# Kernel tuning notes

Hardware: AMD Instinct MI355X
Metric: run time of the kernel (lower is better)

The kernel has to match this reference:

```python
import jax, jax.numpy as jnp
import numpy as np

D_MODEL = 1024
EXPAND = 2
D_INNER = D_MODEL * EXPAND  # 2048
C = 8
B, T = 4, 2048


def setup_inputs() -> dict:
    key = jax.random.key(0)
    ks = jax.random.split(key, 8)
    x = jax.random.normal(ks[0], (B, T, D_MODEL), jnp.float32)
    # omega init: uniform in [a, b] per the torch code
    a = np.log(1.0 / np.exp(np.log(0.999) / C) - 1.0)
    b = np.log(1.0 / np.exp(np.log(0.9) / C) - 1.0)
    omega = (a + (b - a) * jax.random.uniform(ks[1], (1, 1, D_INNER))).astype(jnp.float32)
    s = 0.02
    Win = (jax.random.normal(ks[2], (2 * D_INNER, D_MODEL)) * s).astype(jnp.float32)   # in_proj, no bias
    Wl = (jax.random.normal(ks[3], (D_INNER, D_INNER)) * s).astype(jnp.float32)        # lambda_proj weight
    bl = jnp.zeros((D_INNER,), jnp.float32)                                            # lambda_proj bias
    Wv = (jax.random.normal(ks[4], (D_INNER, D_INNER)) * s).astype(jnp.float32)        # mixer householder-vector proj
    bv = jnp.zeros((D_INNER,), jnp.float32)
    Wout = (jax.random.normal(ks[5], (D_MODEL, D_INNER)) * s).astype(jnp.float32)      # out_proj, no bias
    return dict(x=x, omega=omega, Win=Win, Wl=Wl, bl=bl, Wv=Wv, bv=bv, Wout=Wout)


def reference(x, omega, Win, Wl, bl, Wv, bv, Wout):
    # in_proj then split into (x, z)
    xz = jnp.einsum('btd,ed->bte', x, Win)              # [B,T,2*D_INNER]
    xi, z = jnp.split(xz, 2, axis=-1)                   # each [B,T,D_INNER]
    # lambda gate (computed for all timesteps at once)
    log_lam = -C * jax.nn.softplus(omega) * jax.nn.sigmoid(jnp.einsum('bti,ji->btj', xi, Wl) + bl)
    lam = jnp.exp(log_lam)                              # [B,T,D_INNER]
    # Householder (rank-1, identity activation) mixer vectors, hoisted out of the scan
    v = jnp.einsum('bti,ji->btj', xi, Wv) + bv          # [B,T,D_INNER]

    h0 = xi[:, 0]                                       # [B,D_INNER]

    def step(h_prev, inp):
        x_t, v_t, lam_t = inp
        vh = jnp.sum(v_t * h_prev, axis=-1, keepdims=True)
        vv = jnp.sum(v_t * v_t, axis=-1, keepdims=True)
        Qh = h_prev - 2.0 * v_t * (vh / vv)             # Householder reflection of h
        h = lam_t * Qh + (1.0 - lam_t) * x_t
        return h, h

    xs = (jnp.swapaxes(xi[:, 1:], 0, 1),                # [T-1,B,D_INNER]
          jnp.swapaxes(v[:, 1:], 0, 1),
          jnp.swapaxes(lam[:, 1:], 0, 1))
    _, hs = jax.lax.scan(step, h0, xs)                  # [T-1,B,D_INNER]
    h = jnp.concatenate([h0[:, None], jnp.swapaxes(hs, 0, 1)], axis=1)  # [B,T,D_INNER]

    return jnp.einsum('bti,di->btd', jax.nn.silu(z) * h, Wout)
```

## Files before the change

kernel.cpp:

```cpp
#include <hip/hip_runtime.h>
#include <cstdint>
#include <cstddef>

typedef unsigned short u16;
typedef __attribute__((ext_vector_type(8))) short s8v;
typedef __attribute__((ext_vector_type(4))) float f4v;
typedef __attribute__((ext_vector_type(2))) float f32x2;

#define D_MODEL 1024
#define D_INNER 2048
#define BT      8192
#define TLEN    2048
#define NBATCH  4

struct alignas(8) U16x4 { u16 x, y, z, w; };

__device__ __forceinline__ u16 f2bf(float f) {
  union { float f; unsigned u; } c; c.f = f;
  unsigned r = c.u + 0x7FFFu + ((c.u >> 16) & 1u);
  return (u16)(r >> 16);
}
__device__ __forceinline__ float bf2f(u16 b) {
  union { unsigned u; float f; } c; c.u = ((unsigned)b) << 16;
  return c.f;
}
__device__ __forceinline__ float blo(unsigned u) {
  union { unsigned u; float f; } c; c.u = u << 16; return c.f;
}
__device__ __forceinline__ float bhi(unsigned u) {
  union { unsigned u; float f; } c; c.u = u & 0xffff0000u; return c.f;
}
__device__ __forceinline__ unsigned pkbf(float lo, float hi) {
  union { float f; unsigned u; } a, b; a.f = lo; b.f = hi;
#if __has_builtin(__builtin_amdgcn_perm)
  return __builtin_amdgcn_perm(b.u + 0x8000u, a.u + 0x8000u, 0x07060302u);
#else
  return ((b.u + 0x8000u) & 0xffff0000u) | ((a.u + 0x8000u) >> 16);
#endif
}

#define DPPADD(x, ctrl) \
  ((x) + __builtin_bit_cast(float, __builtin_amdgcn_update_dpp( \
       0, __builtin_bit_cast(int, (x)), (ctrl), 0xF, 0xF, true)))
__device__ __forceinline__ float wave_sum_dpp(float x) {
  x = DPPADD(x, 0x111);
  x = DPPADD(x, 0x112);
  x = DPPADD(x, 0x114);
  x = DPPADD(x, 0x118);
  x = DPPADD(x, 0x142);
  x = DPPADD(x, 0x143);
  return x;
}

__device__ __forceinline__ void glds16(const u16* g, const u16* lds) {
  __builtin_amdgcn_global_load_lds(
      (const __attribute__((address_space(1))) unsigned int*)(uintptr_t)g,
      (__attribute__((address_space(3))) unsigned int*)(unsigned int)(uintptr_t)lds,
      16, 0, 0);
}

template<int EPI>
__global__ __launch_bounds__(256, 2)
void gemm_nt(const u16* __restrict__ A, const u16* __restrict__ B,
             int M, int N, int K,
             float* __restrict__ Cf, u16* __restrict__ Cb, u16* __restrict__ Cb2,
             const float* __restrict__ bias, const float* __restrict__ sfac,
             const float* __restrict__ bias2)
{
  __shared__ u16 lA[128 * 32];
  __shared__ u16 lB[128 * 32];
  const int tid  = threadIdx.x;
  const int wave = tid >> 6, lane = tid & 63;
  const int wm = wave >> 1, wn = wave & 1;
  const int bm0 = blockIdx.y * 128, bn0 = blockIdx.x * 128;

  const int srow = lane >> 2;
  const int scol = (lane & 3) * 8;
  const u16* pa0 = A + (size_t)(bm0 + wave * 32 + srow) * K + scol;
  const u16* pa1 = pa0 + (size_t)16 * K;
  const u16* pb0 = B + (size_t)(bn0 + wave * 32 + srow) * K + scol;
  const u16* pb1 = pb0 + (size_t)16 * K;
  u16* la0 = lA + (wave * 32) * 32;
  u16* la1 = la0 + 16 * 32;
  u16* lb0 = lB + (wave * 32) * 32;
  u16* lb1 = lb0 + 16 * 32;

  const int fr = lane & 15, kq = lane >> 4;
  const u16* fA = lA + (wm * 64 + fr) * 32 + kq * 8;
  const u16* fB = lB + (wn * 64 + fr) * 32 + kq * 8;

  f4v acc[4][4];
  const f4v zf = {0.f, 0.f, 0.f, 0.f};
  for (int i = 0; i < 4; ++i)
    for (int j = 0; j < 4; ++j)
      acc[i][j] = zf;

  for (int k0 = 0; k0 < K; k0 += 32) {
    glds16(pa0 + k0, la0);
    glds16(pa1 + k0, la1);
    glds16(pb0 + k0, lb0);
    glds16(pb1 + k0, lb1);
    __syncthreads();
    s8v af[4], bfv[4];
#pragma unroll
    for (int i = 0; i < 4; ++i) af[i] = *(const s8v*)(fA + i * 16 * 32);
#pragma unroll
    for (int j = 0; j < 4; ++j) bfv[j] = *(const s8v*)(fB + j * 16 * 32);
#pragma unroll
    for (int i = 0; i < 4; ++i)
#pragma unroll
      for (int j = 0; j < 4; ++j)
        acc[i][j] = __builtin_amdgcn_mfma_f32_16x16x32_bf16(af[i], bfv[j], acc[i][j], 0, 0, 0);
    __syncthreads();
  }

#pragma unroll
  for (int i = 0; i < 4; ++i) {
#pragma unroll
    for (int j = 0; j < 4; ++j) {
#pragma unroll
      for (int r = 0; r < 4; ++r) {
        const int gm = bm0 + wm * 64 + i * 16 + kq * 4 + r;
        const int gn = bn0 + wn * 64 + j * 16 + fr;
        const float val = acc[i][j][r];
        if (EPI == 0) {
          if (gn < D_INNER) {
            Cb[(size_t)gm * D_INNER + gn] = f2bf(val);
          } else {
            const float s = val / (1.f + __expf(-val));
            Cb2[(size_t)gm * D_INNER + (gn - D_INNER)] = f2bf(s);
          }
        } else if (EPI == 4) {
          if (gn < D_INNER) {
            const float pre = val + bias[gn];
            const float sig = 1.f / (1.f + __expf(-pre));
            Cf[(size_t)gm * D_INNER + gn] = __expf(sfac[gn] * sig);
          } else {
            Cb[(size_t)gm * D_INNER + (gn - D_INNER)] = f2bf(val + bias2[gn - D_INNER]);
          }
        } else {
          Cf[(size_t)gm * N + gn] = val;
        }
      }
    }
  }
}

__global__ void conv_bf16_kernel(const float* __restrict__ in, u16* __restrict__ out, int n4)
{
  const int i = blockIdx.x * blockDim.x + threadIdx.x;
  if (i >= n4) return;
  const float4 x = ((const float4*)in)[i];
  U16x4 o; o.x = f2bf(x.x); o.y = f2bf(x.y); o.z = f2bf(x.z); o.w = f2bf(x.w);
  ((U16x4*)out)[i] = o;
}

__global__ void sfac_kernel(const float* __restrict__ omega, float* __restrict__ sfac)
{
  const int i = blockIdx.x * blockDim.x + threadIdx.x;
  if (i < D_INNER) sfac[i] = -8.f * log1pf(expf(omega[i]));
}

__global__ __launch_bounds__(256)
void vscale_kernel(u16* __restrict__ v)
{
  const int row  = blockIdx.x * 4 + (threadIdx.x >> 6);
  const int lane = threadIdx.x & 63;
  uint4* p = (uint4*)(v + (size_t)row * D_INNER + lane * 32);
  uint4 a[4];
#pragma unroll
  for (int i = 0; i < 4; ++i) a[i] = p[i];
  float s = 0.f;
#pragma unroll
  for (int i = 0; i < 4; ++i) {
    const unsigned w[4] = {a[i].x, a[i].y, a[i].z, a[i].w};
#pragma unroll
    for (int j = 0; j < 4; ++j) {
      const float f0 = blo(w[j]), f1 = bhi(w[j]);
      s += f0 * f0 + f1 * f1;
    }
  }
  s += __shfl_down(s, 32); s += __shfl_down(s, 16); s += __shfl_down(s, 8);
  s += __shfl_down(s, 4);  s += __shfl_down(s, 2);  s += __shfl_down(s, 1);
  const float sc = sqrtf(2.f / __shfl(s, 0));
#pragma unroll
  for (int i = 0; i < 4; ++i) {
    const unsigned w[4] = {a[i].x, a[i].y, a[i].z, a[i].w};
    unsigned o[4];
#pragma unroll
    for (int j = 0; j < 4; ++j) o[j] = pkbf(blo(w[j]) * sc, bhi(w[j]) * sc);
    uint4 ov; ov.x = o[0]; ov.y = o[1]; ov.z = o[2]; ov.w = o[3];
    p[i] = ov;
  }
}

__global__ __launch_bounds__(256)
void pairprep_kernel(const u16* __restrict__ vs, const float* __restrict__ lam,
                     const u16* __restrict__ xi, u16* __restrict__ w,
                     f32x2* __restrict__ C12)
{
  const int r = blockIdx.x * 4 + (threadIdx.x >> 6);
  const int lane = threadIdx.x & 63;
  const int b = r >> 10;
  const int t = (r & 1023) * 2;
  const size_t o0 = ((size_t)b * TLEN + t) * D_INNER + (size_t)lane * 32;
  const size_t o1 = o0 + D_INNER;
  const uint4*  pv0 = (const uint4*)(vs + o0);
  const uint4*  pv1 = (const uint4*)(vs + o1);
  const uint4*  px0 = (const uint4*)(xi + o0);
  const float4* pl0 = (const float4*)(lam + o0);
  uint4* pw = (uint4*)(w + (size_t)r * D_INNER + (size_t)lane * 32);
  float c1 = 0.f, c2 = 0.f;
#pragma unroll
  for (int i = 0; i < 4; ++i) {
    const uint4 v0 = pv0[i], v1 = pv1[i], x0 = px0[i];
    const float4 la = pl0[2 * i], lb2 = pl0[2 * i + 1];
    const unsigned v0w[4] = {v0.x, v0.y, v0.z, v0.w};
    const unsigned v1w[4] = {v1.x, v1.y, v1.z, v1.w};
    const unsigned x0w[4] = {x0.x, x0.y, x0.z, x0.w};
    const float lf[8] = {la.x, la.y, la.z, la.w, lb2.x, lb2.y, lb2.z, lb2.w};
    unsigned ow[4];
#pragma unroll
    for (int q = 0; q < 4; ++q) {
      const float va = blo(v0w[q]), vb = bhi(v0w[q]);
      const float ua = blo(v1w[q]), ub = bhi(v1w[q]);
      const float xa = blo(x0w[q]), xb = bhi(x0w[q]);
      ow[q] = pkbf(ua * lf[2 * q], ub * lf[2 * q + 1]);
      c1 += blo(ow[q]) * va + bhi(ow[q]) * vb;
      c2 += ua * (1.f - lf[2 * q]) * xa + ub * (1.f - lf[2 * q + 1]) * xb;
    }
    uint4 o; o.x = ow[0]; o.y = ow[1]; o.z = ow[2]; o.w = ow[3];
    pw[i] = o;
  }
  c1 = wave_sum_dpp(c1);
  c2 = wave_sum_dpp(c2);
  if (lane == 63) { f32x2 cc; cc.x = c1; cc.y = c2; C12[r] = cc; }
}

struct Pair {
  uint4 v0, v1, w, x0, x1, z0, z1;
  float4 l0a, l0b, l1a, l1b;
  f32x2 c;
};

__global__ __launch_bounds__(256, 1)
void scan2_kernel(const u16* __restrict__ xi, const u16* __restrict__ sz,
                  const u16* __restrict__ vs, const float* __restrict__ lam,
                  const u16* __restrict__ whalf, const f32x2* __restrict__ C12,
                  u16* __restrict__ gh)
{
  const int b = blockIdx.x, tid = threadIdx.x;
  const int wave = tid >> 6, lane = tid & 63;
  const size_t base = (size_t)b * TLEN * D_INNER + (size_t)tid * 8;
  const size_t wb0  = (size_t)(b * 1024) * D_INNER + (size_t)tid * 8;
  const int cb0 = b * 1024;
  __shared__ __attribute__((aligned(16))) float rP[2][4], rQ[2][4];

  auto load_pair = [&](int t) {
    Pair p;
    const size_t o0 = base + (size_t)t * D_INNER;
    const size_t o1 = o0 + D_INNER;
    p.v0 = *(const uint4*)(vs + o0);
    p.v1 = *(const uint4*)(vs + o1);
    p.w  = *(const uint4*)(whalf + wb0 + (size_t)(t >> 1) * D_INNER);
    p.x0 = *(const uint4*)(xi + o0);
    p.x1 = *(const uint4*)(xi + o1);
    p.z0 = *(const uint4*)(sz + o0);
    p.z1 = *(const uint4*)(sz + o1);
    const float4* l0p = (const float4*)(lam + o0);
    p.l0a = l0p[0]; p.l0b = l0p[1];
    const float4* l1p = (const float4*)(lam + o1);
    p.l1a = l1p[0]; p.l1b = l1p[1];
    p.c = C12[cb0 + (t >> 1)];
    return p;
  };

  float h[8];
  {
    const uint4 x0 = *(const uint4*)(xi + base);
    const uint4 z0 = *(const uint4*)(sz + base);
    const unsigned xw[4] = {x0.x, x0.y, x0.z, x0.w};
    const unsigned zw[4] = {z0.x, z0.y, z0.z, z0.w};
    unsigned ow[4];
#pragma unroll
    for (int p = 0; p < 4; ++p) {
      h[2*p]   = blo(xw[p]);
      h[2*p+1] = bhi(xw[p]);
      ow[p] = pkbf(blo(zw[p]) * h[2*p], bhi(zw[p]) * h[2*p+1]);
    }
    uint4 out; out.x = ow[0]; out.y = ow[1]; out.z = ow[2]; out.w = ow[3];
    *(uint4*)(gh + base) = out;
  }

  {
    const size_t o = base + D_INNER;
    const uint4 v1v = *(const uint4*)(vs + o);
    const uint4 x1v = *(const uint4*)(xi + o);
    const uint4 z1v = *(const uint4*)(sz + o);
    const float4* lp = (const float4*)(lam + o);
    const float4 la = lp[0], lb2 = lp[1];
    const unsigned vw[4] = {v1v.x, v1v.y, v1v.z, v1v.w};
    float vf[8];
    float P0 = 0.f, P1 = 0.f;
#pragma unroll
    for (int p = 0; p < 4; ++p) {
      vf[2*p]   = blo(vw[p]);
      vf[2*p+1] = bhi(vw[p]);
      P0 = __builtin_fmaf(vf[2*p],   h[2*p],   P0);
      P1 = __builtin_fmaf(vf[2*p+1], h[2*p+1], P1);
    }
    float P = wave_sum_dpp(P0 + P1);
    if (lane == 63) rP[0][wave] = P;
    asm volatile("s_waitcnt lgkmcnt(0)\n\ts_barrier" ::: "memory");
    const float4 sp = *(const float4*)rP[0];
    const float a = (sp.x + sp.y) + (sp.z + sp.w);
    const float lf[8] = {la.x, la.y, la.z, la.w, lb2.x, lb2.y, lb2.z, lb2.w};
    const unsigned xw[4] = {x1v.x, x1v.y, x1v.z, x1v.w};
    const unsigned zw[4] = {z1v.x, z1v.y, z1v.z, z1v.w};
    unsigned ow[4];
#pragma unroll
    for (int p = 0; p < 4; ++p) {
      const float X0 = blo(xw[p]), X1 = bhi(xw[p]);
      const float t0 = __builtin_fmaf(vf[2*p],   -a, h[2*p]);
      const float t1 = __builtin_fmaf(vf[2*p+1], -a, h[2*p+1]);
      h[2*p]   = __builtin_fmaf(lf[2*p],   t0 - X0, X0);
      h[2*p+1] = __builtin_fmaf(lf[2*p+1], t1 - X1, X1);
      ow[p] = pkbf(blo(zw[p]) * h[2*p], bhi(zw[p]) * h[2*p+1]);
    }
    uint4 out; out.x = ow[0]; out.y = ow[1]; out.z = ow[2]; out.w = ow[3];
    *(uint4*)(gh + o) = out;
  }

  auto round = [&](const Pair& p, int t) {
    const int par = (t >> 1) & 1;
    const unsigned vw[4] = {p.v0.x, p.v0.y, p.v0.z, p.v0.w};
    const unsigned ww[4] = {p.w.x, p.w.y, p.w.z, p.w.w};
    float vf[8];
    float P0 = 0.f, P1 = 0.f, Q0 = 0.f, Q1 = 0.f;
#pragma unroll
    for (int q = 0; q < 4; ++q) {
      vf[2*q]   = blo(vw[q]);
      vf[2*q+1] = bhi(vw[q]);
      const float wa = blo(ww[q]), wb = bhi(ww[q]);
      P0 = __builtin_fmaf(vf[2*q],   h[2*q],   P0);
      P1 = __builtin_fmaf(vf[2*q+1], h[2*q+1], P1);
      Q0 = __builtin_fmaf(wa, h[2*q],   Q0);
      Q1 = __builtin_fmaf(wb, h[2*q+1], Q1);
    }
    float P = wave_sum_dpp(P0 + P1);
    float Q = wave_sum_dpp(Q0 + Q1);
    if (lane == 63) { rP[par][wave] = P; rQ[par][wave] = Q; }
    asm volatile("s_waitcnt lgkmcnt(0)\n\ts_barrier" ::: "memory");
    const float4 sp = *(const float4*)rP[par];
    const float4 sq = *(const float4*)rQ[par];
    const float a0 = (sp.x + sp.y) + (sp.z + sp.w);
    const float a1 = __builtin_fmaf(-a0, p.c.x, (sq.x + sq.y) + (sq.z + sq.w) + p.c.y);
    const float lf0[8] = {p.l0a.x, p.l0a.y, p.l0a.z, p.l0a.w,
                          p.l0b.x, p.l0b.y, p.l0b.z, p.l0b.w};
    const float lf1[8] = {p.l1a.x, p.l1a.y, p.l1a.z, p.l1a.w,
                          p.l1b.x, p.l1b.y, p.l1b.z, p.l1b.w};
    const unsigned v1w[4] = {p.v1.x, p.v1.y, p.v1.z, p.v1.w};
    const unsigned xw0[4] = {p.x0.x, p.x0.y, p.x0.z, p.x0.w};
    const unsigned xw1[4] = {p.x1.x, p.x1.y, p.x1.z, p.x1.w};
    const unsigned zw0[4] = {p.z0.x, p.z0.y, p.z0.z, p.z0.w};
    const unsigned zw1[4] = {p.z1.x, p.z1.y, p.z1.z, p.z1.w};
    unsigned ow0[4], ow1[4];
#pragma unroll
    for (int q = 0; q < 4; ++q) {
      const float A0 = blo(xw0[q]), A1 = bhi(xw0[q]);
      const float B0 = blo(xw1[q]), B1 = bhi(xw1[q]);
      float t0 = __builtin_fmaf(vf[2*q],   -a0, h[2*q]);
      float t1 = __builtin_fmaf(vf[2*q+1], -a0, h[2*q+1]);
      t0 = __builtin_fmaf(lf0[2*q],   t0 - A0, A0);
      t1 = __builtin_fmaf(lf0[2*q+1], t1 - A1, A1);
      ow0[q] = pkbf(blo(zw0[q]) * t0, bhi(zw0[q]) * t1);
      const float u0 = __builtin_fmaf(blo(v1w[q]), -a1, t0);
      const float u1 = __builtin_fmaf(bhi(v1w[q]), -a1, t1);
      h[2*q]   = __builtin_fmaf(lf1[2*q],   u0 - B0, B0);
      h[2*q+1] = __builtin_fmaf(lf1[2*q+1], u1 - B1, B1);
      ow1[q] = pkbf(blo(zw1[q]) * h[2*q], bhi(zw1[q]) * h[2*q+1]);
    }
    const size_t oo = base + (size_t)t * D_INNER;
    uint4 o0; o0.x = ow0[0]; o0.y = ow0[1]; o0.z = ow0[2]; o0.w = ow0[3];
    uint4 o1; o1.x = ow1[0]; o1.y = ow1[1]; o1.z = ow1[2]; o1.w = ow1[3];
    *(uint4*)(gh + oo) = o0;
    *(uint4*)(gh + oo + D_INNER) = o1;
  };

  Pair A = load_pair(2);
  __builtin_amdgcn_sched_barrier(0);
  Pair B = load_pair(4);
  __builtin_amdgcn_sched_barrier(0);
  for (int t = 2; t <= 2038; t += 4) {
    Pair An = load_pair(t + 4);
    __builtin_amdgcn_sched_barrier(0);
    round(A, t);
    A = An;
    Pair Bn = load_pair(t + 6);
    __builtin_amdgcn_sched_barrier(0);
    round(B, t + 2);
    B = Bn;
  }
  {
    Pair An = load_pair(2046);
    __builtin_amdgcn_sched_barrier(0);
    round(A, 2042);
    round(B, 2044);
    round(An, 2046);
  }
}

extern "C" void kernel_launch(void* const* d_in, const int* in_sizes, int n_in,
                              void* d_out, int out_size, void* d_ws, size_t ws_size,
                              hipStream_t stream)
{
  const float* x     = (const float*)d_in[0];
  const float* omega = (const float*)d_in[1];
  const float* Win   = (const float*)d_in[2];
  const float* Wl    = (const float*)d_in[3];
  const float* bl    = (const float*)d_in[4];
  const float* Wv    = (const float*)d_in[5];
  const float* bv    = (const float*)d_in[6];
  const float* Wout  = (const float*)d_in[7];
  float* out = (float*)d_out;
  (void)in_sizes; (void)n_in; (void)out_size; (void)ws_size;

  size_t off = 0;
  auto carve = [&](size_t bytes) -> void* {
    void* r = (char*)d_ws + off;
    off += (bytes + 255) & ~(size_t)255;
    return r;
  };
  u16*  x_bf    = (u16*)carve((size_t)BT * D_MODEL * 2);
  u16*  Win_bf  = (u16*)carve((size_t)2 * D_INNER * D_MODEL * 2);
  u16*  Wl_bf   = (u16*)carve((size_t)D_INNER * D_INNER * 2);
  u16*  Wv_bf   = (u16*)carve((size_t)D_INNER * D_INNER * 2);
  u16*  Wout_bf = (u16*)carve((size_t)D_MODEL * D_INNER * 2);
  u16*  xi_bf   = (u16*)carve((size_t)BT * D_INNER * 2);
  u16*  sz_bf   = (u16*)carve((size_t)BT * D_INNER * 2);
  u16*  v_bf    = (u16*)carve((size_t)BT * D_INNER * 2);
  u16*  gh_bf   = (u16*)carve((size_t)BT * D_INNER * 2);
  float* lam    = (float*)carve((size_t)BT * D_INNER * 4);
  float* sfac   = (float*)carve((size_t)D_INNER * 4);
  f32x2* C12    = (f32x2*)carve((size_t)(BT / 2) * 8);
  u16*  whalf   = x_bf;

  conv_bf16_kernel<<<(BT * D_MODEL / 4 + 255) / 256, 256, 0, stream>>>(x, x_bf, BT * D_MODEL / 4);
  conv_bf16_kernel<<<(2 * D_INNER * D_MODEL / 4 + 255) / 256, 256, 0, stream>>>(Win, Win_bf, 2 * D_INNER * D_MODEL / 4);
  conv_bf16_kernel<<<(D_INNER * D_INNER / 4 + 255) / 256, 256, 0, stream>>>(Wl, Wl_bf, D_INNER * D_INNER / 4);
  conv_bf16_kernel<<<(D_INNER * D_INNER / 4 + 255) / 256, 256, 0, stream>>>(Wv, Wv_bf, D_INNER * D_INNER / 4);
  conv_bf16_kernel<<<(D_MODEL * D_INNER / 4 + 255) / 256, 256, 0, stream>>>(Wout, Wout_bf, D_MODEL * D_INNER / 4);
  sfac_kernel<<<(D_INNER + 255) / 256, 256, 0, stream>>>(omega, sfac);

  gemm_nt<0><<<dim3(4096 / 128, BT / 128), 256, 0, stream>>>(
      x_bf, Win_bf, BT, 4096, D_MODEL, nullptr, xi_bf, sz_bf, nullptr, nullptr, nullptr);
  gemm_nt<4><<<dim3(4096 / 128, BT / 128), 256, 0, stream>>>(
      xi_bf, Wl_bf, BT, 4096, D_INNER, lam, v_bf, nullptr, bl, sfac, bv);
  vscale_kernel<<<BT / 4, 256, 0, stream>>>(v_bf);
  pairprep_kernel<<<BT / 2 / 4, 256, 0, stream>>>(v_bf, lam, xi_bf, whalf, C12);
  scan2_kernel<<<NBATCH, 256, 0, stream>>>(xi_bf, sz_bf, v_bf, lam, whalf, C12, gh_bf);
  gemm_nt<3><<<dim3(D_MODEL / 128, BT / 128), 256, 0, stream>>>(
      gh_bf, Wout_bf, BT, D_MODEL, D_INNER, out, nullptr, nullptr, nullptr, nullptr, nullptr);
}
```

Baseline: 1.265 ms.

## Unroll Householder scan to four steps per barrier with precomputed quad coefficients

Replaces the pairwise scan with a four-step blocked recurrence. A prep kernel precomputes the lambda-weighted v vectors and the scalar coupling coefficients for each quad, so the sequential scan needs only one block barrier per four timesteps. The scan block also grows to 512 threads with 4 elements per thread, which makes each step shorter. In exchange the prep kernel does more work and writes three weight rows per quad, and the scan reads more data per step.

Result: slower. 1.472 ms (+16.3%).

```diff
diff --git a/kernel.cpp b/kernel.cpp
--- a/kernel.cpp
+++ b/kernel.cpp
@@ -5,13 +5,14 @@
 typedef unsigned short u16;
 typedef __attribute__((ext_vector_type(8))) short s8v;
 typedef __attribute__((ext_vector_type(4))) float f4v;
-typedef __attribute__((ext_vector_type(2))) float f32x2;
 
 #define D_MODEL 1024
 #define D_INNER 2048
 #define BT      8192
 #define TLEN    2048
 #define NBATCH  4
+#define QSLOT   512
+#define NQUAD   511
 
 struct alignas(8) U16x4 { u16 x, y, z, w; };
 
@@ -19,10 +20,6 @@
   union { float f; unsigned u; } c; c.f = f;
   unsigned r = c.u + 0x7FFFu + ((c.u >> 16) & 1u);
   return (u16)(r >> 16);
-}
-__device__ __forceinline__ float bf2f(u16 b) {
-  union { unsigned u; float f; } c; c.u = ((unsigned)b) << 16;
-  return c.f;
 }
 __device__ __forceinline__ float blo(unsigned u) {
   union { unsigned u; float f; } c; c.u = u << 16; return c.f;
@@ -195,219 +192,262 @@
 }
 
 __global__ __launch_bounds__(256)
-void pairprep_kernel(const u16* __restrict__ vs, const float* __restrict__ lam,
-                     const u16* __restrict__ xi, u16* __restrict__ w,
-                     f32x2* __restrict__ C12)
+void quadprep_kernel(const u16* __restrict__ vs, const float* __restrict__ lam,
+                     const u16* __restrict__ xi, u16* __restrict__ wq,
+                     float4* __restrict__ cf)
 {
   const int r = blockIdx.x * 4 + (threadIdx.x >> 6);
   const int lane = threadIdx.x & 63;
-  const int b = r >> 10;
-  const int t = (r & 1023) * 2;
-  const size_t o0 = ((size_t)b * TLEN + t) * D_INNER + (size_t)lane * 32;
-  const size_t o1 = o0 + D_INNER;
-  const uint4*  pv0 = (const uint4*)(vs + o0);
-  const uint4*  pv1 = (const uint4*)(vs + o1);
-  const uint4*  px0 = (const uint4*)(xi + o0);
-  const float4* pl0 = (const float4*)(lam + o0);
-  uint4* pw = (uint4*)(w + (size_t)r * D_INNER + (size_t)lane * 32);
-  float c1 = 0.f, c2 = 0.f;
+  const int b = r >> 9;
+  const int q = r & (QSLOT - 1);
+  if (q >= NQUAD) return;
+  const int t0 = 4 * q + 1;
+  const size_t e = ((size_t)b * TLEN + t0) * D_INNER + (size_t)lane * 32;
+  u16* w2p = wq + ((size_t)r * 3 + 0) * D_INNER + (size_t)lane * 32;
+  u16* w3p = wq + ((size_t)r * 3 + 1) * D_INNER + (size_t)lane * 32;
+  u16* w4p = wq + ((size_t)r * 3 + 2) * D_INNER + (size_t)lane * 32;
+
+  float c21 = 0, c31 = 0, c32 = 0, c41 = 0, c42 = 0, c43 = 0;
+  float d2 = 0, d3 = 0, d4 = 0;
+
 #pragma unroll
   for (int i = 0; i < 4; ++i) {
-    const uint4 v0 = pv0[i], v1 = pv1[i], x0 = px0[i];
-    const float4 la = pl0[2 * i], lb2 = pl0[2 * i + 1];
-    const unsigned v0w[4] = {v0.x, v0.y, v0.z, v0.w};
+    const size_t o = e + i * 8;
+    const uint4 v1 = *(const uint4*)(vs + o);
+    const uint4 v2 = *(const uint4*)(vs + o + D_INNER);
+    const uint4 v3 = *(const uint4*)(vs + o + 2 * D_INNER);
+    const uint4 v4 = *(const uint4*)(vs + o + 3 * D_INNER);
+    const uint4 x1 = *(const uint4*)(xi + o);
+    const uint4 x2 = *(const uint4*)(xi + o + D_INNER);
+    const uint4 x3 = *(const uint4*)(xi + o + 2 * D_INNER);
+    const float4* l1p = (const float4*)(lam + o);
+    const float4* l2p = (const float4*)(lam + o + D_INNER);
+    const float4* l3p = (const float4*)(lam + o + 2 * D_INNER);
+    const float4 l1a4 = l1p[0], l1b4 = l1p[1];
+    const float4 l2a4 = l2p[0], l2b4 = l2p[1];
+    const float4 l3a4 = l3p[0], l3b4 = l3p[1];
+    const float lf1[8] = {l1a4.x, l1a4.y, l1a4.z, l1a4.w, l1b4.x, l1b4.y, l1b4.z, l1b4.w};
+    const float lf2[8] = {l2a4.x, l2a4.y, l2a4.z, l2a4.w, l2b4.x, l2b4.y, l2b4.z, l2b4.w};
+    const float lf3[8] = {l3a4.x, l3a4.y, l3a4.z, l3a4.w, l3b4.x, l3b4.y, l3b4.z, l3b4.w};
     const unsigned v1w[4] = {v1.x, v1.y, v1.z, v1.w};
-    const unsigned x0w[4] = {x0.x, x0.y, x0.z, x0.w};
-    const float lf[8] = {la.x, la.y, la.z, la.w, lb2.x, lb2.y, lb2.z, lb2.w};
-    unsigned ow[4];
-#pragma unroll
-    for (int q = 0; q < 4; ++q) {
-      const float va = blo(v0w[q]), vb = bhi(v0w[q]);
-      const float ua = blo(v1w[q]), ub = bhi(v1w[q]);
-      const float xa = blo(x0w[q]), xb = bhi(x0w[q]);
-      ow[q] = pkbf(ua * lf[2 * q], ub * lf[2 * q + 1]);
-      c1 += blo(ow[q]) * va + bhi(ow[q]) * vb;
-      c2 += ua * (1.f - lf[2 * q]) * xa + ub * (1.f - lf[2 * q + 1]) * xb;
-    }
-    uint4 o; o.x = ow[0]; o.y = ow[1]; o.z = ow[2]; o.w = ow[3];
-    pw[i] = o;
-  }
-  c1 = wave_sum_dpp(c1);
-  c2 = wave_sum_dpp(c2);
-  if (lane == 63) { f32x2 cc; cc.x = c1; cc.y = c2; C12[r] = cc; }
-}
-
-struct Pair {
-  uint4 v0, v1, w, x0, x1, z0, z1;
-  float4 l0a, l0b, l1a, l1b;
-  f32x2 c;
+    const unsigned v2w[4] = {v2.x, v2.y, v2.z, v2.w};
+    const unsigned v3w[4] = {v3.x, v3.y, v3.z, v3.w};
+    const unsigned v4w[4] = {v4.x, v4.y, v4.z, v4.w};
+    const unsigned x1w[4] = {x1.x, x1.y, x1.z, x1.w};
+    const unsigned x2w[4] = {x2.x, x2.y, x2.z, x2.w};
+    const unsigned x3w[4] = {x3.x, x3.y, x3.z, x3.w};
+    unsigned ow2[4], ow3[4], ow4[4];
+#pragma unroll
+    for (int k = 0; k < 4; ++k) {
+      const float v1a = blo(v1w[k]), v1b = bhi(v1w[k]);
+      const float v2a = blo(v2w[k]), v2b = bhi(v2w[k]);
+      const float v3a = blo(v3w[k]), v3b = bhi(v3w[k]);
+      const float v4a = blo(v4w[k]), v4b = bhi(v4w[k]);
+      const float l1a = lf1[2*k], l1b = lf1[2*k+1];
+      const float l2a = lf2[2*k], l2b = lf2[2*k+1];
+      const float l3a = lf3[2*k], l3b = lf3[2*k+1];
+      const float u1a = (1.f - l1a) * blo(x1w[k]), u1b = (1.f - l1b) * bhi(x1w[k]);
+      const float u2a = (1.f - l2a) * blo(x2w[k]), u2b = (1.f - l2b) * bhi(x2w[k]);
+      const float u3a = (1.f - l3a) * blo(x3w[k]), u3b = (1.f - l3b) * bhi(x3w[k]);
+      const float p2a = v2a * l1a, p2b = v2b * l1b;
+      ow2[k] = pkbf(p2a, p2b);
+      c21 += blo(ow2[k]) * v1a + bhi(ow2[k]) * v1b;
+      d2  += v2a * u1a + v2b * u1b;
+      const float p3a = v3a * l2a, p3b = v3b * l2b;
+      c32 += p3a * v2a + p3b * v2b;
+      d3  += p3a * u1a + p3b * u1b + v3a * u2a + v3b * u2b;
+      const float w3a = p3a * l1a, w3b = p3b * l1b;
+      ow3[k] = pkbf(w3a, w3b);
+      c31 += blo(ow3[k]) * v1a + bhi(ow3[k]) * v1b;
+      const float p4a = v4a * l3a, p4b = v4b * l3b;
+      c43 += p4a * v3a + p4b * v3b;
+      const float q4a = p4a * l2a, q4b = p4b * l2b;
+      c42 += q4a * v2a + q4b * v2b;
+      d4  += q4a * u1a + q4b * u1b + p4a * u2a + p4b * u2b + v4a * u3a + v4b * u3b;
+      const float w4a = q4a * l1a, w4b = q4b * l1b;
+      ow4[k] = pkbf(w4a, w4b);
+      c41 += blo(ow4[k]) * v1a + bhi(ow4[k]) * v1b;
+    }
+    uint4 s2; s2.x = ow2[0]; s2.y = ow2[1]; s2.z = ow2[2]; s2.w = ow2[3];
+    uint4 s3; s3.x = ow3[0]; s3.y = ow3[1]; s3.z = ow3[2]; s3.w = ow3[3];
+    uint4 s4; s4.x = ow4[0]; s4.y = ow4[1]; s4.z = ow4[2]; s4.w = ow4[3];
+    *(uint4*)(w2p + i * 8) = s2;
+    *(uint4*)(w3p + i * 8) = s3;
+    *(uint4*)(w4p + i * 8) = s4;
+  }
+  c21 = wave_sum_dpp(c21); c31 = wave_sum_dpp(c31); c32 = wave_sum_dpp(c32);
+  c41 = wave_sum_dpp(c41); c42 = wave_sum_dpp(c42); c43 = wave_sum_dpp(c43);
+  d2 = wave_sum_dpp(d2); d3 = wave_sum_dpp(d3); d4 = wave_sum_dpp(d4);
+  if (lane == 63) {
+    float4 a; a.x = c21; a.y = c31; a.z = c32; a.w = c41;
+    float4 bq; bq.x = c42; bq.y = c43; bq.z = d2; bq.w = d3;
+    float4 cc; cc.x = d4; cc.y = 0.f; cc.z = 0.f; cc.w = 0.f;
+    cf[(size_t)r * 3 + 0] = a;
+    cf[(size_t)r * 3 + 1] = bq;
+    cf[(size_t)r * 3 + 2] = cc;
+  }
+}
+
+struct Quad {
+  uint2 w2, w3, w4;
+  uint2 v1, v2, v3, v4;
+  uint2 x1, x2, x3, x4;
+  uint2 z1, z2, z3, z4;
+  float4 l1, l2, l3, l4;
+  float4 c0, c1, c2;
 };
 
-__global__ __launch_bounds__(256, 1)
-void scan2_kernel(const u16* __restrict__ xi, const u16* __restrict__ sz,
+__global__ __launch_bounds__(512, 2)
+void scan4_kernel(const u16* __restrict__ xi, const u16* __restrict__ sz,
                   const u16* __restrict__ vs, const float* __restrict__ lam,
-                  const u16* __restrict__ whalf, const f32x2* __restrict__ C12,
+                  const u16* __restrict__ wq, const float4* __restrict__ cf,
                   u16* __restrict__ gh)
 {
   const int b = blockIdx.x, tid = threadIdx.x;
   const int wave = tid >> 6, lane = tid & 63;
-  const size_t base = (size_t)b * TLEN * D_INNER + (size_t)tid * 8;
-  const size_t wb0  = (size_t)(b * 1024) * D_INNER + (size_t)tid * 8;
-  const int cb0 = b * 1024;
-  __shared__ __attribute__((aligned(16))) float rP[2][4], rQ[2][4];
-
-  auto load_pair = [&](int t) {
-    Pair p;
-    const size_t o0 = base + (size_t)t * D_INNER;
-    const size_t o1 = o0 + D_INNER;
-    p.v0 = *(const uint4*)(vs + o0);
-    p.v1 = *(const uint4*)(vs + o1);
-    p.w  = *(const uint4*)(whalf + wb0 + (size_t)(t >> 1) * D_INNER);
-    p.x0 = *(const uint4*)(xi + o0);
-    p.x1 = *(const uint4*)(xi + o1);
-    p.z0 = *(const uint4*)(sz + o0);
-    p.z1 = *(const uint4*)(sz + o1);
-    const float4* l0p = (const float4*)(lam + o0);
-    p.l0a = l0p[0]; p.l0b = l0p[1];
-    const float4* l1p = (const float4*)(lam + o1);
-    p.l1a = l1p[0]; p.l1b = l1p[1];
-    p.c = C12[cb0 + (t >> 1)];
+  const size_t base = (size_t)b * TLEN * D_INNER + (size_t)tid * 4;
+  __shared__ __attribute__((aligned(16))) float sS[2][4][8];
+
+  auto load_quad = [&](int q) {
+    Quad p;
+    const size_t e1 = base + (size_t)(4 * q + 1) * D_INNER;
+    p.v1 = *(const uint2*)(vs + e1);
+    p.v2 = *(const uint2*)(vs + e1 + D_INNER);
+    p.v3 = *(const uint2*)(vs + e1 + 2 * D_INNER);
+    p.v4 = *(const uint2*)(vs + e1 + 3 * D_INNER);
+    p.x1 = *(const uint2*)(xi + e1);
+    p.x2 = *(const uint2*)(xi + e1 + D_INNER);
+    p.x3 = *(const uint2*)(xi + e1 + 2 * D_INNER);
+    p.x4 = *(const uint2*)(xi + e1 + 3 * D_INNER);
+    p.z1 = *(const uint2*)(sz + e1);
+    p.z2 = *(const uint2*)(sz + e1 + D_INNER);
+    p.z3 = *(const uint2*)(sz + e1 + 2 * D_INNER);
+    p.z4 = *(const uint2*)(sz + e1 + 3 * D_INNER);
+    p.l1 = *(const float4*)(lam + e1);
+    p.l2 = *(const float4*)(lam + e1 + D_INNER);
+    p.l3 = *(const float4*)(lam + e1 + 2 * D_INNER);
+    p.l4 = *(const float4*)(lam + e1 + 3 * D_INNER);
+    const size_t wr = ((size_t)(b * QSLOT + q) * 3) * D_INNER + (size_t)tid * 4;
+    p.w2 = *(const uint2*)(wq + wr);
+    p.w3 = *(const uint2*)(wq + wr + D_INNER);
+    p.w4 = *(const uint2*)(wq + wr + 2 * D_INNER);
+    const float4* cp = cf + (size_t)(b * QSLOT + q) * 3;
+    p.c0 = cp[0]; p.c1 = cp[1]; p.c2 = cp[2];
     return p;
   };
 
-  float h[8];
+  float h[4];
   {
-    const uint4 x0 = *(const uint4*)(xi + base);
-    const uint4 z0 = *(const uint4*)(sz + base);
-    const unsigned xw[4] = {x0.x, x0.y, x0.z, x0.w};
-    const unsigned zw[4] = {z0.x, z0.y, z0.z, z0.w};
-    unsigned ow[4];
-#pragma unroll
-    for (int p = 0; p < 4; ++p) {
-      h[2*p]   = blo(xw[p]);
-      h[2*p+1] = bhi(xw[p]);
-      ow[p] = pkbf(blo(zw[p]) * h[2*p], bhi(zw[p]) * h[2*p+1]);
-    }
-    uint4 out; out.x = ow[0]; out.y = ow[1]; out.z = ow[2]; out.w = ow[3];
-    *(uint4*)(gh + base) = out;
-  }
-
+    const uint2 x0 = *(const uint2*)(xi + base);
+    const uint2 z0 = *(const uint2*)(sz + base);
+    h[0] = blo(x0.x); h[1] = bhi(x0.x); h[2] = blo(x0.y); h[3] = bhi(x0.y);
+    uint2 ov;
+    ov.x = pkbf(blo(z0.x) * h[0], bhi(z0.x) * h[1]);
+    ov.y = pkbf(blo(z0.y) * h[2], bhi(z0.y) * h[3]);
+    *(uint2*)(gh + base) = ov;
+  }
+
+  auto step = [&](uint2 vv, float4 lv, uint2 xv, uint2 zv, float s, size_t off) {
+    const float vf[4] = {blo(vv.x), bhi(vv.x), blo(vv.y), bhi(vv.y)};
+    const float xf[4] = {blo(xv.x), bhi(xv.x), blo(xv.y), bhi(xv.y)};
+    const float lf[4] = {lv.x, lv.y, lv.z, lv.w};
+#pragma unroll
+    for (int k = 0; k < 4; ++k) {
+      const float t_ = __builtin_fmaf(vf[k], -s, h[k]);
+      h[k] = __builtin_fmaf(lf[k], t_ - xf[k], xf[k]);
+    }
+    uint2 ov;
+    ov.x = pkbf(blo(zv.x) * h[0], bhi(zv.x) * h[1]);
+    ov.y = pkbf(blo(zv.y) * h[2], bhi(zv.y) * h[3]);
+    *(uint2*)(gh + off) = ov;
+  };
+
+  auto round = [&](const Quad& p, int q) {
+    const int par = q & 1;
+    const float v1f[4] = {blo(p.v1.x), bhi(p.v1.x), blo(p.v1.y), bhi(p.v1.y)};
+    const float w2f[4] = {blo(p.w2.x), bhi(p.w2.x), blo(p.w2.y), bhi(p.w2.y)};
+    const float w3f[4] = {blo(p.w3.x), bhi(p.w3.x), blo(p.w3.y), bhi(p.w3.y)};
+    const float w4f[4] = {blo(p.w4.x), bhi(p.w4.x), blo(p.w4.y), bhi(p.w4.y)};
+    float P1 = 0.f, P2 = 0.f, P3 = 0.f, P4 = 0.f;
+#pragma unroll
+    for (int k = 0; k < 4; ++k) {
+      P1 = __builtin_fmaf(v1f[k], h[k], P1);
+      P2 = __builtin_fmaf(w2f[k], h[k], P2);
+      P3 = __builtin_fmaf(w3f[k], h[k], P3);
+      P4 = __builtin_fmaf(w4f[k], h[k], P4);
+    }
+    P1 = wave_sum_dpp(P1); P2 = wave_sum_dpp(P2);
+    P3 = wave_sum_dpp(P3); P4 = wave_sum_dpp(P4);
+    if (lane == 63) {
+      sS[par][0][wave] = P1; sS[par][1][wave] = P2;
+      sS[par][2][wave] = P3; sS[par][3][wave] = P4;
+    }
+    asm volatile("s_waitcnt lgkmcnt(0)\n\ts_barrier" ::: "memory");
+    float S[4];
+#pragma unroll
+    for (int j = 0; j < 4; ++j) {
+      const float4 pa = *(const float4*)&sS[par][j][0];
+      const float4 pb = *(const float4*)&sS[par][j][4];
+      S[j] = ((pa.x + pa.y) + (pa.z + pa.w)) + ((pb.x + pb.y) + (pb.z + pb.w));
+    }
+    const float c21 = p.c0.x, c31 = p.c0.y, c32 = p.c0.z, c41 = p.c0.w;
+    const float c42 = p.c1.x, c43 = p.c1.y, d2 = p.c1.z, d3 = p.c1.w;
+    const float d4 = p.c2.x;
+    const float s1 = S[0];
+    const float s2 = __builtin_fmaf(-c21, s1, S[1] + d2);
+    const float s3 = __builtin_fmaf(-c32, s2, __builtin_fmaf(-c31, s1, S[2] + d3));
+    const float s4 = __builtin_fmaf(-c43, s3,
+                      __builtin_fmaf(-c42, s2, __builtin_fmaf(-c41, s1, S[3] + d4)));
+    const size_t e1 = base + (size_t)(4 * q + 1) * D_INNER;
+    step(p.v1, p.l1, p.x1, p.z1, s1, e1);
+    step(p.v2, p.l2, p.x2, p.z2, s2, e1 + D_INNER);
+    step(p.v3, p.l3, p.x3, p.z3, s3, e1 + 2 * D_INNER);
+    step(p.v4, p.l4, p.x4, p.z4, s4, e1 + 3 * D_INNER);
+  };
+
+  auto solo = [&](int t, int par) {
+    const size_t o = base + (size_t)t * D_INNER;
+    const uint2 vv = *(const uint2*)(vs + o);
+    const uint2 xv = *(const uint2*)(xi + o);
+    const uint2 zv = *(const uint2*)(sz + o);
+    const float4 lv = *(const float4*)(lam + o);
+    const float vf[4] = {blo(vv.x), bhi(vv.x), blo(vv.y), bhi(vv.y)};
+    float P = 0.f;
+#pragma unroll
+    for (int k = 0; k < 4; ++k) P = __builtin_fmaf(vf[k], h[k], P);
+    P = wave_sum_dpp(P);
+    if (lane == 63) sS[par][0][wave] = P;
+    asm volatile("s_waitcnt lgkmcnt(0)\n\ts_barrier" ::: "memory");
+    const float4 pa = *(const float4*)&sS[par][0][0];
+    const float4 pb = *(const float4*)&sS[par][0][4];
+    const float s = ((pa.x + pa.y) + (pa.z + pa.w)) + ((pb.x + pb.y) + (pb.z + pb.w));
+    step(vv, lv, xv, zv, s, o);
+  };
+
+  Quad A = load_quad(0);
+  __builtin_amdgcn_sched_barrier(0);
+  Quad B = load_quad(1);
+  __builtin_amdgcn_sched_barrier(0);
+  for (int q = 0; q <= 507; q += 2) {
+    Quad An = load_quad(q + 2);
+    __builtin_amdgcn_sched_barrier(0);
+    round(A, q);
+    A = An;
+    Quad Bn = load_quad(q + 3);
+    __builtin_amdgcn_sched_barrier(0);
+    round(B, q + 1);
+    B = Bn;
+  }
   {
-    const size_t o = base + D_INNER;
-    const uint4 v1v = *(const uint4*)(vs + o);
-    const uint4 x1v = *(const uint4*)(xi + o);
-    const uint4 z1v = *(const uint4*)(sz + o);
-    const float4* lp = (const float4*)(lam + o);
-    const float4 la = lp[0], lb2 = lp[1];
-    const unsigned vw[4] = {v1v.x, v1v.y, v1v.z, v1v.w};
-    float vf[8];
-    float P0 = 0.f, P1 = 0.f;
-#pragma unroll
-    for (int p = 0; p < 4; ++p) {
-      vf[2*p]   = blo(vw[p]);
-      vf[2*p+1] = bhi(vw[p]);
-      P0 = __builtin_fmaf(vf[2*p],   h[2*p],   P0);
-      P1 = __builtin_fmaf(vf[2*p+1], h[2*p+1], P1);
-    }
-    float P = wave_sum_dpp(P0 + P1);
-    if (lane == 63) rP[0][wave] = P;
-    asm volatile("s_waitcnt lgkmcnt(0)\n\ts_barrier" ::: "memory");
-    const float4 sp = *(const float4*)rP[0];
-    const float a = (sp.x + sp.y) + (sp.z + sp.w);
-    const float lf[8] = {la.x, la.y, la.z, la.w, lb2.x, lb2.y, lb2.z, lb2.w};
-    const unsigned xw[4] = {x1v.x, x1v.y, x1v.z, x1v.w};
-    const unsigned zw[4] = {z1v.x, z1v.y, z1v.z, z1v.w};
-    unsigned ow[4];
-#pragma unroll
-    for (int p = 0; p < 4; ++p) {
-      const float X0 = blo(xw[p]), X1 = bhi(xw[p]);
-      const float t0 = __builtin_fmaf(vf[2*p],   -a, h[2*p]);
-      const float t1 = __builtin_fmaf(vf[2*p+1], -a, h[2*p+1]);
-      h[2*p]   = __builtin_fmaf(lf[2*p],   t0 - X0, X0);
-      h[2*p+1] = __builtin_fmaf(lf[2*p+1], t1 - X1, X1);
-      ow[p] = pkbf(blo(zw[p]) * h[2*p], bhi(zw[p]) * h[2*p+1]);
-    }
-    uint4 out; out.x = ow[0]; out.y = ow[1]; out.z = ow[2]; out.w = ow[3];
-    *(uint4*)(gh + o) = out;
-  }
-
-  auto round = [&](const Pair& p, int t) {
-    const int par = (t >> 1) & 1;
-    const unsigned vw[4] = {p.v0.x, p.v0.y, p.v0.z, p.v0.w};
-    const unsigned ww[4] = {p.w.x, p.w.y, p.w.z, p.w.w};
-    float vf[8];
-    float P0 = 0.f, P1 = 0.f, Q0 = 0.f, Q1 = 0.f;
-#pragma unroll
-    for (int q = 0; q < 4; ++q) {
-      vf[2*q]   = blo(vw[q]);
-      vf[2*q+1] = bhi(vw[q]);
-      const float wa = blo(ww[q]), wb = bhi(ww[q]);
-      P0 = __builtin_fmaf(vf[2*q],   h[2*q],   P0);
-      P1 = __builtin_fmaf(vf[2*q+1], h[2*q+1], P1);
-      Q0 = __builtin_fmaf(wa, h[2*q],   Q0);
-      Q1 = __builtin_fmaf(wb, h[2*q+1], Q1);
-    }
-    float P = wave_sum_dpp(P0 + P1);
-    float Q = wave_sum_dpp(Q0 + Q1);
-    if (lane == 63) { rP[par][wave] = P; rQ[par][wave] = Q; }
-    asm volatile("s_waitcnt lgkmcnt(0)\n\ts_barrier" ::: "memory");
-    const float4 sp = *(const float4*)rP[par];
-    const float4 sq = *(const float4*)rQ[par];
-    const float a0 = (sp.x + sp.y) + (sp.z + sp.w);
-    const float a1 = __builtin_fmaf(-a0, p.c.x, (sq.x + sq.y) + (sq.z + sq.w) + p.c.y);
-    const float lf0[8] = {p.l0a.x, p.l0a.y, p.l0a.z, p.l0a.w,
-                          p.l0b.x, p.l0b.y, p.l0b.z, p.l0b.w};
-    const float lf1[8] = {p.l1a.x, p.l1a.y, p.l1a.z, p.l1a.w,
-                          p.l1b.x, p.l1b.y, p.l1b.z, p.l1b.w};
-    const unsigned v1w[4] = {p.v1.x, p.v1.y, p.v1.z, p.v1.w};
-    const unsigned xw0[4] = {p.x0.x, p.x0.y, p.x0.z, p.x0.w};
-    const unsigned xw1[4] = {p.x1.x, p.x1.y, p.x1.z, p.x1.w};
-    const unsigned zw0[4] = {p.z0.x, p.z0.y, p.z0.z, p.z0.w};
-    const unsigned zw1[4] = {p.z1.x, p.z1.y, p.z1.z, p.z1.w};
-    unsigned ow0[4], ow1[4];
-#pragma unroll
-    for (int q = 0; q < 4; ++q) {
-      const float A0 = blo(xw0[q]), A1 = bhi(xw0[q]);
-      const float B0 = blo(xw1[q]), B1 = bhi(xw1[q]);
-      float t0 = __builtin_fmaf(vf[2*q],   -a0, h[2*q]);
-      float t1 = __builtin_fmaf(vf[2*q+1], -a0, h[2*q+1]);
-      t0 = __builtin_fmaf(lf0[2*q],   t0 - A0, A0);
-      t1 = __builtin_fmaf(lf0[2*q+1], t1 - A1, A1);
-      ow0[q] = pkbf(blo(zw0[q]) * t0, bhi(zw0[q]) * t1);
-      const float u0 = __builtin_fmaf(blo(v1w[q]), -a1, t0);
-      const float u1 = __builtin_fmaf(bhi(v1w[q]), -a1, t1);
-      h[2*q]   = __builtin_fmaf(lf1[2*q],   u0 - B0, B0);
-      h[2*q+1] = __builtin_fmaf(lf1[2*q+1], u1 - B1, B1);
-      ow1[q] = pkbf(blo(zw1[q]) * h[2*q], bhi(zw1[q]) * h[2*q+1]);
-    }
-    const size_t oo = base + (size_t)t * D_INNER;
-    uint4 o0; o0.x = ow0[0]; o0.y = ow0[1]; o0.z = ow0[2]; o0.w = ow0[3];
-    uint4 o1; o1.x = ow1[0]; o1.y = ow1[1]; o1.z = ow1[2]; o1.w = ow1[3];
-    *(uint4*)(gh + oo) = o0;
-    *(uint4*)(gh + oo + D_INNER) = o1;
-  };
-
-  Pair A = load_pair(2);
-  __builtin_amdgcn_sched_barrier(0);
-  Pair B = load_pair(4);
-  __builtin_amdgcn_sched_barrier(0);
-  for (int t = 2; t <= 2038; t += 4) {
-    Pair An = load_pair(t + 4);
+    Quad An = load_quad(510);
     __builtin_amdgcn_sched_barrier(0);
-    round(A, t);
-    A = An;
-    Pair Bn = load_pair(t + 6);
-    __builtin_amdgcn_sched_barrier(0);
-    round(B, t + 2);
-    B = Bn;
-  }
-  {
-    Pair An = load_pair(2046);
-    __builtin_amdgcn_sched_barrier(0);
-    round(A, 2042);
-    round(B, 2044);
-    round(An, 2046);
-  }
+    round(A, 508);
+    round(B, 509);
+    round(An, 510);
+  }
+  solo(2045, 1);
+  solo(2046, 0);
+  solo(2047, 1);
 }
 
 extern "C" void kernel_launch(void* const* d_in, const int* in_sizes, int n_in,
@@ -442,8 +482,8 @@
   u16*  gh_bf   = (u16*)carve((size_t)BT * D_INNER * 2);
   float* lam    = (float*)carve((size_t)BT * D_INNER * 4);
   float* sfac   = (float*)carve((size_t)D_INNER * 4);
-  f32x2* C12    = (f32x2*)carve((size_t)(BT / 2) * 8);
-  u16*  whalf   = x_bf;
+  float4* cf    = (float4*)carve((size_t)NBATCH * QSLOT * 3 * 16);
+  u16*  wquad   = x_bf;
 
   conv_bf16_kernel<<<(BT * D_MODEL / 4 + 255) / 256, 256, 0, stream>>>(x, x_bf, BT * D_MODEL / 4);
   conv_bf16_kernel<<<(2 * D_INNER * D_MODEL / 4 + 255) / 256, 256, 0, stream>>>(Win, Win_bf, 2 * D_INNER * D_MODEL / 4);
@@ -457,8 +497,8 @@
   gemm_nt<4><<<dim3(4096 / 128, BT / 128), 256, 0, stream>>>(
       xi_bf, Wl_bf, BT, 4096, D_INNER, lam, v_bf, nullptr, bl, sfac, bv);
   vscale_kernel<<<BT / 4, 256, 0, stream>>>(v_bf);
-  pairprep_kernel<<<BT / 2 / 4, 256, 0, stream>>>(v_bf, lam, xi_bf, whalf, C12);
-  scan2_kernel<<<NBATCH, 256, 0, stream>>>(xi_bf, sz_bf, v_bf, lam, whalf, C12, gh_bf);
+  quadprep_kernel<<<NBATCH * QSLOT / 4, 256, 0, stream>>>(v_bf, lam, xi_bf, wquad, cf);
+  scan4_kernel<<<NBATCH, 512, 0, stream>>>(xi_bf, sz_bf, v_bf, lam, wquad, cf, gh_bf);
   gemm_nt<3><<<dim3(D_MODEL / 128, BT / 128), 256, 0, stream>>>(
       gh_bf, Wout_bf, BT, D_MODEL, D_INNER, out, nullptr, nullptr, nullptr, nullptr, nullptr);
 }
```
